# Kernel optimization log

Measured on AMD Instinct MI355X. Metric: run time of the kernel, lower is better.

## Reference

```python
import jax, jax.numpy as jnp
import numpy as np

N_NODES = 100000
N_EDGES = 1600000
IN_DIM = 128
OUT_DIM = 64


def setup_inputs() -> dict:
    key = jax.random.key(0)
    k1, k2, k3, k4, k5 = jax.random.split(key, 5)
    return {
        "h_init": jax.random.normal(k1, (N_NODES, IN_DIM), dtype=jnp.float32),
        "W1": jax.random.normal(k2, (OUT_DIM, IN_DIM), dtype=jnp.float32),
        "a": jax.random.normal(k3, (1, OUT_DIM), dtype=jnp.float32),
        "src": jax.random.randint(k4, (N_EDGES,), 0, N_NODES, dtype=jnp.int64)
        if jax.config.jax_enable_x64 else jax.random.randint(k4, (N_EDGES,), 0, N_NODES, dtype=jnp.int32),
        "dst": jax.random.randint(k5, (N_EDGES,), 0, N_NODES, dtype=jnp.int32),
    }


def reference(h_init, W1, a, src, dst):
    N = h_init.shape[0]
    # node projection: [N, out_dim]
    h = h_init @ W1.T
    # per-edge diff feature: dst minus src (DGL edges.dst['h'] - edges.src['h'])
    diff = h[dst] - h[src]                       # [E, out_dim]
    e = jnp.tanh(diff @ a[0])                    # [E] edge attention logit
    # segment softmax over incoming edges of each destination node
    seg_max = jax.ops.segment_max(e, dst, num_segments=N)   # [N]
    ex = jnp.exp(e - seg_max[dst])               # [E]
    denom = jax.ops.segment_sum(ex, dst, num_segments=N)    # [N]
    alpha = ex / denom[dst]                      # [E]
    # weighted sum of diff features per destination node
    h_diff = jax.ops.segment_sum(alpha[:, None] * diff, dst, num_segments=N)  # [N, out_dim]
    return jax.nn.relu(h + h_diff)
```

## Files before the change

### kernel.cpp

```cpp
#include <hip/hip_runtime.h>
#include <hip/hip_fp16.h>

#define N_NODES 100000
#define N_EDGES 1600000
#define IN_DIM 128
#define OUT_DIM 64

#define NBUCK 391
#define MAXB 4608
#define CUR_STRIDE 16

#define BIN_NBLK 250
#define BIN_CHUNK 6400

#define PROJ_BLKS 1563
#define PB_GRID (PROJ_BLKS + BIN_NBLK)

#define SG_THREADS 1024

typedef short short8 __attribute__((ext_vector_type(8)));
typedef float f32x4 __attribute__((ext_vector_type(4)));

__device__ __forceinline__ short bf16_trunc(float x) {
  return (short)(__float_as_uint(x) >> 16);
}
__device__ __forceinline__ float bf16_tof(short s) {
  return __uint_as_float(((unsigned)(unsigned short)s) << 16);
}
__device__ __forceinline__ float edge_ex(float p) {
  float t2 = __expf(2.f * p);
  float th = 1.f - 2.f * __builtin_amdgcn_rcpf(t2 + 1.f);
  return __expf(th);
}

__global__ __launch_bounds__(256) void fused_pb_kernel(
    const float* __restrict__ h_init, const float* __restrict__ W1,
    const float* __restrict__ a, const int* __restrict__ src,
    const int* __restrict__ dst, float* __restrict__ h,
    __half* __restrict__ h16, float* __restrict__ ha,
    int* __restrict__ bucket_cursor, unsigned int* __restrict__ pairs) {
  __shared__ __align__(16) char smem[16 * 64 * 8 * 2 * sizeof(short)];

  int idx = blockIdx.x;
  int q7 = idx / 7, r7 = idx % 7;
  if (r7 == 3 && q7 < BIN_NBLK) {
    int* hst = (int*)smem;
    int* cur = hst + NBUCK;
    for (int i = threadIdx.x; i < NBUCK; i += 256) hst[i] = 0;
    __syncthreads();
    int beg = q7 * BIN_CHUNK;
    int end = beg + BIN_CHUNK;
    for (int e = beg + threadIdx.x; e < end; e += 256)
      atomicAdd(&hst[dst[e] >> 8], 1);
    __syncthreads();
    for (int i = threadIdx.x; i < NBUCK; i += 256) {
      int c = hst[i];
      cur[i] = (c > 0) ? atomicAdd(&bucket_cursor[i * CUR_STRIDE], c) + i * MAXB
                       : 0;
    }
    __syncthreads();
    for (int e = beg + threadIdx.x; e < end; e += 256) {
      int d = dst[e];
      int pos = atomicAdd(&cur[d >> 8], 1);
      pairs[pos] = ((unsigned int)src[e] << 8) | (unsigned int)(d & 255);
    }
    return;
  }

  int pb = idx - min(q7 + (r7 > 3 ? 1 : 0), BIN_NBLK);
  short* whi = (short*)smem;
  short* wlo = whi + 16 * 64 * 8;

  for (int i2 = threadIdx.x; i2 < 16 * 64; i2 += 256) {
    int f = i2 >> 6;
    int l = i2 & 63;
    int kc = f >> 2, ot = f & 3;
    const float* wsrc =
        W1 + (ot * 16 + (l & 15)) * IN_DIM + kc * 32 + (l >> 4) * 8;
    short hi[8], lo[8];
#pragma unroll
    for (int j = 0; j < 8; j++) {
      float x = wsrc[j];
      short hv = bf16_trunc(x);
      hi[j] = hv;
      lo[j] = bf16_trunc(x - bf16_tof(hv));
    }
    *(short8*)&whi[i2 * 8] = *(const short8*)hi;
    *(short8*)&wlo[i2 * 8] = *(const short8*)lo;
  }

  int row0 = pb * 64;
  int w = threadIdx.x >> 6;
  int l = threadIdx.x & 63;
  int m = l & 15;
  int q = l >> 4;

  int arow = row0 + w * 16 + m;
  if (arow >= N_NODES) arow = N_NODES - 1;
  const float* xsrc = h_init + (size_t)arow * IN_DIM + q * 8;

  short8 ahi[4], alo[4];
#pragma unroll
  for (int kc = 0; kc < 4; kc++) {
    float xv[8];
    *(float4*)&xv[0] = *(const float4*)(xsrc + kc * 32);
    *(float4*)&xv[4] = *(const float4*)(xsrc + kc * 32 + 4);
    short hi[8], lo[8];
#pragma unroll
    for (int j = 0; j < 8; j++) {
      short hv = bf16_trunc(xv[j]);
      hi[j] = hv;
      lo[j] = bf16_trunc(xv[j] - bf16_tof(hv));
    }
    ahi[kc] = *(const short8*)hi;
    alo[kc] = *(const short8*)lo;
  }
  __syncthreads();

  f32x4 acc[4] = {{0.f, 0.f, 0.f, 0.f},
                  {0.f, 0.f, 0.f, 0.f},
                  {0.f, 0.f, 0.f, 0.f},
                  {0.f, 0.f, 0.f, 0.f}};

#pragma unroll
  for (int kc = 0; kc < 4; kc++) {
#pragma unroll
    for (int ot = 0; ot < 4; ot++) {
      int base = (((kc << 2) | ot) * 64 + l) * 8;
      short8 bhi = *(const short8*)&whi[base];
      short8 blo = *(const short8*)&wlo[base];
      acc[ot] = __builtin_amdgcn_mfma_f32_16x16x32_bf16(ahi[kc], bhi, acc[ot],
                                                        0, 0, 0);
      acc[ot] = __builtin_amdgcn_mfma_f32_16x16x32_bf16(ahi[kc], blo, acc[ot],
                                                        0, 0, 0);
      acc[ot] = __builtin_amdgcn_mfma_f32_16x16x32_bf16(alo[kc], bhi, acc[ot],
                                                        0, 0, 0);
    }
  }

  float pa[4] = {0.f, 0.f, 0.f, 0.f};
#pragma unroll
  for (int ot = 0; ot < 4; ot++) {
    float aval = a[ot * 16 + m];
#pragma unroll
    for (int r = 0; r < 4; r++) pa[r] += acc[ot][r] * aval;
  }
  int rowb = row0 + w * 16 + q * 4;
#pragma unroll
  for (int r = 0; r < 4; r++) {
    int row = rowb + r;
    if (row < N_NODES) {
#pragma unroll
      for (int ot = 0; ot < 4; ot++) {
        h[(size_t)row * OUT_DIM + ot * 16 + m] = acc[ot][r];
        h16[(size_t)row * OUT_DIM + ot * 16 + m] = __float2half(acc[ot][r]);
      }
    }
  }
#pragma unroll
  for (int r = 0; r < 4; r++) {
    pa[r] += __shfl_xor(pa[r], 1);
    pa[r] += __shfl_xor(pa[r], 2);
    pa[r] += __shfl_xor(pa[r], 4);
    pa[r] += __shfl_xor(pa[r], 8);
  }
  if (m == 0) {
#pragma unroll
    for (int r = 0; r < 4; r++) {
      int row = rowb + r;
      if (row < N_NODES) ha[row] = pa[r];
    }
  }
}

__global__ __launch_bounds__(SG_THREADS) void sortgather_kernel(
    const float* __restrict__ h, const __half* __restrict__ h16,
    const float* __restrict__ ha, const int* __restrict__ bucket_cursor,
    const unsigned int* __restrict__ pairs, float* __restrict__ out) {
  __shared__ unsigned int plds[MAXB];
  __shared__ int2 slds[MAXB];
  __shared__ float had[256];
  __shared__ int hist[256];
  __shared__ int scn[256];
  __shared__ int cur[256];
  int b = blockIdx.x;
  int t = threadIdx.x;
  int node0 = b << 8;
  int cnt = min(bucket_cursor[b * CUR_STRIDE], MAXB);

  if (t < 256) {
    int node = node0 + t;
    had[t] = (node < N_NODES) ? ha[node] : 0.f;
    hist[t] = 0;
  }
  __syncthreads();
  for (int i = t; i < cnt; i += SG_THREADS) {
    unsigned int p = pairs[(size_t)b * MAXB + i];
    plds[i] = p;
    atomicAdd(&hist[p & 255u], 1);
  }
  __syncthreads();
  int v = (t < 256) ? hist[t] : 0;
  if (t < 256) scn[t] = v;
  __syncthreads();
  for (int off = 1; off < 256; off <<= 1) {
    int u = (t >= off && t < 256) ? scn[t - off] : 0;
    __syncthreads();
    if (t < 256) scn[t] += u;
    __syncthreads();
  }
  if (t < 256) cur[t] = scn[t] - v;
  __syncthreads();
  for (int i = t; i < cnt; i += SG_THREADS) {
    unsigned int p = plds[i];
    int nl = (int)(p & 255u);
    int s = (int)(p >> 8);
    float ex = edge_ex(had[nl] - ha[s]);
    int pos = atomicAdd(&cur[nl], 1);
    slds[pos] = make_int2(s << 7, __float_as_int(ex));
  }
  __syncthreads();

  int wv = t >> 6;
  int lane = t & 63;
  int g = lane >> 3;
  int l8 = lane & 7;
  const char* h16b = (const char*)h16;
  const float4* h4 = (const float4*)h;
  float4* o4 = (float4*)out;

  for (int nl = wv; nl < 256; nl += 16) {
    int node = node0 + nl;
    if (node >= N_NODES) break;
    int endp = scn[nl];
    int begp = endp - hist[nl];
    float4 hd0 = h4[(size_t)node * (OUT_DIM / 4) + l8 * 2];
    float4 hd1 = h4[(size_t)node * (OUT_DIM / 4) + l8 * 2 + 1];
    float acc[8] = {0.f, 0.f, 0.f, 0.f, 0.f, 0.f, 0.f, 0.f};
    float den = 0.f;
    int last = endp - 1;

    for (int base = begp + g * 4; base < endp; base += 32) {
      int2 e[4];
      float exv[4];
#pragma unroll
      for (int k = 0; k < 4; k++) {
        int i = base + k;
        e[k] = slds[i < endp ? i : last];
        exv[k] = (i < endp) ? __int_as_float(e[k].y) : 0.f;
      }
      uint4 uv[4];
#pragma unroll
      for (int k = 0; k < 4; k++)
        uv[k] = *(const uint4*)(h16b + e[k].x + (l8 << 4));
#pragma unroll
      for (int k = 0; k < 4; k++) {
        union {
          uint4 u;
          __half hh[8];
        } U;
        U.u = uv[k];
        float ex = exv[k];
        den += ex;
#pragma unroll
        for (int j = 0; j < 8; j++)
          acc[j] = fmaf(__half2float(U.hh[j]), ex, acc[j]);
      }
    }

#pragma unroll
    for (int j = 0; j < 8; j++) {
      acc[j] += __shfl_xor(acc[j], 8);
      acc[j] += __shfl_xor(acc[j], 16);
      acc[j] += __shfl_xor(acc[j], 32);
    }
    den += __shfl_xor(den, 8);
    den += __shfl_xor(den, 16);
    den += __shfl_xor(den, 32);

    if (g == 0) {
      bool has = den > 0.f;
      float inv = has ? __builtin_amdgcn_rcpf(den) : 0.f;
      float4 r0, r1;
      r0.x = fmaxf(has ? 2.f * hd0.x - acc[0] * inv : hd0.x, 0.f);
      r0.y = fmaxf(has ? 2.f * hd0.y - acc[1] * inv : hd0.y, 0.f);
      r0.z = fmaxf(has ? 2.f * hd0.z - acc[2] * inv : hd0.z, 0.f);
      r0.w = fmaxf(has ? 2.f * hd0.w - acc[3] * inv : hd0.w, 0.f);
      r1.x = fmaxf(has ? 2.f * hd1.x - acc[4] * inv : hd1.x, 0.f);
      r1.y = fmaxf(has ? 2.f * hd1.y - acc[5] * inv : hd1.y, 0.f);
      r1.z = fmaxf(has ? 2.f * hd1.z - acc[6] * inv : hd1.z, 0.f);
      r1.w = fmaxf(has ? 2.f * hd1.w - acc[7] * inv : hd1.w, 0.f);
      o4[(size_t)node * (OUT_DIM / 4) + l8 * 2] = r0;
      o4[(size_t)node * (OUT_DIM / 4) + l8 * 2 + 1] = r1;
    }
  }
}

extern "C" void kernel_launch(void* const* d_in, const int* in_sizes, int n_in,
                              void* d_out, int out_size, void* d_ws,
                              size_t ws_size, hipStream_t stream) {
  const float* h_init = (const float*)d_in[0];
  const float* W1 = (const float*)d_in[1];
  const float* a = (const float*)d_in[2];
  const int* src = (const int*)d_in[3];
  const int* dst = (const int*)d_in[4];
  float* out = (float*)d_out;

  float* h = (float*)d_ws;
  __half* h16 = (__half*)(h + (size_t)N_NODES * OUT_DIM);
  float* ha = (float*)(h16 + (size_t)N_NODES * OUT_DIM);
  unsigned int* pairs = (unsigned int*)(ha + N_NODES);
  int* bucket_cursor = (int*)(pairs + (size_t)NBUCK * MAXB);

  hipMemsetAsync(bucket_cursor, 0, NBUCK * CUR_STRIDE * sizeof(int), stream);
  fused_pb_kernel<<<PB_GRID, 256, 0, stream>>>(h_init, W1, a, src, dst, h, h16,
                                               ha, bucket_cursor, pairs);
  sortgather_kernel<<<NBUCK, SG_THREADS, 0, stream>>>(h, h16, ha, bucket_cursor,
                                                      pairs, out);
}
```

Measured before the change: 214.9 us.

## Split projection and binning kernels, halve bucket size to 128 nodes

Moves the edge-binning work out of the fused projection kernel into a separate 1024-thread bin/scatter kernel that caches dst in LDS. Halves the bucket granularity (782 buckets of 128 nodes, 512-thread sortgather blocks) to raise block count and occupancy in the gather stage. It also changes the gather loop so each lane group handles interleaved edges, and stores the shifted source offset directly. Splitting adds a kernel launch and loses the overlap of binning with projection, and the smaller MAXB2 capacity raises overflow risk for skewed buckets.

```diff
diff --git a/kernel.cpp b/kernel.cpp
--- a/kernel.cpp
+++ b/kernel.cpp
@@ -6,17 +6,17 @@
 #define IN_DIM 128
 #define OUT_DIM 64
 
-#define NBUCK 391
-#define MAXB 4608
+#define PROJ_BLKS 1563
+
+#define NB2 782
+#define MAXB2 2560
 #define CUR_STRIDE 16
 
 #define BIN_NBLK 250
 #define BIN_CHUNK 6400
-
-#define PROJ_BLKS 1563
-#define PB_GRID (PROJ_BLKS + BIN_NBLK)
-
-#define SG_THREADS 1024
+#define BIN_THREADS 1024
+
+#define SG_THREADS 512
 
 typedef short short8 __attribute__((ext_vector_type(8)));
 typedef float f32x4 __attribute__((ext_vector_type(4)));
@@ -33,47 +33,16 @@
   return __expf(th);
 }
 
-__global__ __launch_bounds__(256) void fused_pb_kernel(
+__global__ __launch_bounds__(256) void fat1_kernel(
     const float* __restrict__ h_init, const float* __restrict__ W1,
-    const float* __restrict__ a, const int* __restrict__ src,
-    const int* __restrict__ dst, float* __restrict__ h,
-    __half* __restrict__ h16, float* __restrict__ ha,
-    int* __restrict__ bucket_cursor, unsigned int* __restrict__ pairs) {
-  __shared__ __align__(16) char smem[16 * 64 * 8 * 2 * sizeof(short)];
-
-  int idx = blockIdx.x;
-  int q7 = idx / 7, r7 = idx % 7;
-  if (r7 == 3 && q7 < BIN_NBLK) {
-    int* hst = (int*)smem;
-    int* cur = hst + NBUCK;
-    for (int i = threadIdx.x; i < NBUCK; i += 256) hst[i] = 0;
-    __syncthreads();
-    int beg = q7 * BIN_CHUNK;
-    int end = beg + BIN_CHUNK;
-    for (int e = beg + threadIdx.x; e < end; e += 256)
-      atomicAdd(&hst[dst[e] >> 8], 1);
-    __syncthreads();
-    for (int i = threadIdx.x; i < NBUCK; i += 256) {
-      int c = hst[i];
-      cur[i] = (c > 0) ? atomicAdd(&bucket_cursor[i * CUR_STRIDE], c) + i * MAXB
-                       : 0;
-    }
-    __syncthreads();
-    for (int e = beg + threadIdx.x; e < end; e += 256) {
-      int d = dst[e];
-      int pos = atomicAdd(&cur[d >> 8], 1);
-      pairs[pos] = ((unsigned int)src[e] << 8) | (unsigned int)(d & 255);
-    }
-    return;
-  }
-
-  int pb = idx - min(q7 + (r7 > 3 ? 1 : 0), BIN_NBLK);
-  short* whi = (short*)smem;
-  short* wlo = whi + 16 * 64 * 8;
-
-  for (int i2 = threadIdx.x; i2 < 16 * 64; i2 += 256) {
-    int f = i2 >> 6;
-    int l = i2 & 63;
+    const float* __restrict__ a, float* __restrict__ h,
+    __half* __restrict__ h16, float* __restrict__ ha) {
+  __shared__ short whi[16 * 64 * 8];
+  __shared__ short wlo[16 * 64 * 8];
+
+  for (int idx = threadIdx.x; idx < 16 * 64; idx += 256) {
+    int f = idx >> 6;
+    int l = idx & 63;
     int kc = f >> 2, ot = f & 3;
     const float* wsrc =
         W1 + (ot * 16 + (l & 15)) * IN_DIM + kc * 32 + (l >> 4) * 8;
@@ -85,11 +54,11 @@
       hi[j] = hv;
       lo[j] = bf16_trunc(x - bf16_tof(hv));
     }
-    *(short8*)&whi[i2 * 8] = *(const short8*)hi;
-    *(short8*)&wlo[i2 * 8] = *(const short8*)lo;
-  }
-
-  int row0 = pb * 64;
+    *(short8*)&whi[idx * 8] = *(const short8*)hi;
+    *(short8*)&wlo[idx * 8] = *(const short8*)lo;
+  }
+
+  int row0 = blockIdx.x * 64;
   int w = threadIdx.x >> 6;
   int l = threadIdx.x & 63;
   int m = l & 15;
@@ -173,51 +142,80 @@
   }
 }
 
+__global__ __launch_bounds__(BIN_THREADS) void bin_scatter_kernel(
+    const int* __restrict__ src, const int* __restrict__ dst,
+    int* __restrict__ bucket_cursor, unsigned int* __restrict__ pairs) {
+  __shared__ int hst[NB2];
+  __shared__ int cur[NB2];
+  __shared__ int dlds[BIN_CHUNK];
+  int t = threadIdx.x;
+  for (int i = t; i < NB2; i += BIN_THREADS) hst[i] = 0;
+  __syncthreads();
+  int beg = blockIdx.x * BIN_CHUNK;
+  for (int e = t; e < BIN_CHUNK; e += BIN_THREADS) {
+    int d = dst[beg + e];
+    dlds[e] = d;
+    atomicAdd(&hst[d >> 7], 1);
+  }
+  __syncthreads();
+  for (int i = t; i < NB2; i += BIN_THREADS) {
+    int c = hst[i];
+    cur[i] =
+        (c > 0) ? atomicAdd(&bucket_cursor[i * CUR_STRIDE], c) + i * MAXB2 : 0;
+  }
+  __syncthreads();
+  for (int e = t; e < BIN_CHUNK; e += BIN_THREADS) {
+    int d = dlds[e];
+    int pos = atomicAdd(&cur[d >> 7], 1);
+    pairs[pos] = ((unsigned int)src[beg + e] << 7) | (unsigned int)(d & 127);
+  }
+}
+
 __global__ __launch_bounds__(SG_THREADS) void sortgather_kernel(
     const float* __restrict__ h, const __half* __restrict__ h16,
     const float* __restrict__ ha, const int* __restrict__ bucket_cursor,
     const unsigned int* __restrict__ pairs, float* __restrict__ out) {
-  __shared__ unsigned int plds[MAXB];
-  __shared__ int2 slds[MAXB];
-  __shared__ float had[256];
-  __shared__ int hist[256];
-  __shared__ int scn[256];
-  __shared__ int cur[256];
+  __shared__ unsigned int plds[MAXB2];
+  __shared__ int2 slds[MAXB2];
+  __shared__ float had[128];
+  __shared__ int hist[128];
+  __shared__ int scn[128];
+  __shared__ int cur[128];
   int b = blockIdx.x;
   int t = threadIdx.x;
-  int node0 = b << 8;
-  int cnt = min(bucket_cursor[b * CUR_STRIDE], MAXB);
-
-  if (t < 256) {
+  int node0 = b << 7;
+  int cnt = min(bucket_cursor[b * CUR_STRIDE], MAXB2);
+
+  if (t < 128) {
     int node = node0 + t;
     had[t] = (node < N_NODES) ? ha[node] : 0.f;
     hist[t] = 0;
   }
   __syncthreads();
   for (int i = t; i < cnt; i += SG_THREADS) {
-    unsigned int p = pairs[(size_t)b * MAXB + i];
+    unsigned int p = pairs[(size_t)b * MAXB2 + i];
     plds[i] = p;
-    atomicAdd(&hist[p & 255u], 1);
-  }
-  __syncthreads();
-  int v = (t < 256) ? hist[t] : 0;
-  if (t < 256) scn[t] = v;
-  __syncthreads();
-  for (int off = 1; off < 256; off <<= 1) {
-    int u = (t >= off && t < 256) ? scn[t - off] : 0;
+    atomicAdd(&hist[p & 127u], 1);
+  }
+  __syncthreads();
+  int v = (t < 128) ? hist[t] : 0;
+  if (t < 128) scn[t] = v;
+  __syncthreads();
+  for (int off = 1; off < 128; off <<= 1) {
+    int u = (t >= off && t < 128) ? scn[t - off] : 0;
     __syncthreads();
-    if (t < 256) scn[t] += u;
+    if (t < 128) scn[t] += u;
     __syncthreads();
   }
-  if (t < 256) cur[t] = scn[t] - v;
+  if (t < 128) cur[t] = scn[t] - v;
   __syncthreads();
   for (int i = t; i < cnt; i += SG_THREADS) {
     unsigned int p = plds[i];
-    int nl = (int)(p & 255u);
-    int s = (int)(p >> 8);
-    float ex = edge_ex(had[nl] - ha[s]);
+    int nl = (int)(p & 127u);
+    int sb = (int)(p & 0xFFFFFF80u);
+    float ex = edge_ex(had[nl] - ha[sb >> 7]);
     int pos = atomicAdd(&cur[nl], 1);
-    slds[pos] = make_int2(s << 7, __float_as_int(ex));
+    slds[pos] = make_int2(sb, __float_as_int(ex));
   }
   __syncthreads();
 
@@ -229,7 +227,7 @@
   const float4* h4 = (const float4*)h;
   float4* o4 = (float4*)out;
 
-  for (int nl = wv; nl < 256; nl += 16) {
+  for (int nl = wv; nl < 128; nl += 8) {
     int node = node0 + nl;
     if (node >= N_NODES) break;
     int endp = scn[nl];
@@ -240,12 +238,12 @@
     float den = 0.f;
     int last = endp - 1;
 
-    for (int base = begp + g * 4; base < endp; base += 32) {
+    for (int i0 = begp + g; i0 < endp; i0 += 32) {
       int2 e[4];
       float exv[4];
 #pragma unroll
       for (int k = 0; k < 4; k++) {
-        int i = base + k;
+        int i = i0 + k * 8;
         e[k] = slds[i < endp ? i : last];
         exv[k] = (i < endp) ? __int_as_float(e[k].y) : 0.f;
       }
@@ -310,11 +308,13 @@
   __half* h16 = (__half*)(h + (size_t)N_NODES * OUT_DIM);
   float* ha = (float*)(h16 + (size_t)N_NODES * OUT_DIM);
   unsigned int* pairs = (unsigned int*)(ha + N_NODES);
-  int* bucket_cursor = (int*)(pairs + (size_t)NBUCK * MAXB);
-
-  hipMemsetAsync(bucket_cursor, 0, NBUCK * CUR_STRIDE * sizeof(int), stream);
-  fused_pb_kernel<<<PB_GRID, 256, 0, stream>>>(h_init, W1, a, src, dst, h, h16,
-                                               ha, bucket_cursor, pairs);
-  sortgather_kernel<<<NBUCK, SG_THREADS, 0, stream>>>(h, h16, ha, bucket_cursor,
-                                                      pairs, out);
-}
+  int* bucket_cursor = (int*)(pairs + (size_t)NB2 * MAXB2);
+
+  hipMemsetAsync(bucket_cursor, 0, NB2 * CUR_STRIDE * sizeof(int), stream);
+  fat1_kernel<<<PROJ_BLKS, 256, 0, stream>>>(h_init, W1, a, h, h16, ha);
+  bin_scatter_kernel<<<BIN_NBLK, BIN_THREADS, 0, stream>>>(src, dst,
+                                                           bucket_cursor,
+                                                           pairs);
+  sortgather_kernel<<<NB2, SG_THREADS, 0, stream>>>(h, h16, ha, bucket_cursor,
+                                                    pairs, out);
+}
```

After: 204.7 us. 4.7% less time.
